# Kernel tuning notes

Measured on AMD Instinct MI355X. Metric: run time of the kernel, lower is better.

Reference implementation:

```python
import jax, jax.numpy as jnp
import numpy as np

N = 100000


def _gcn_conv(x, edge_index, W, b):
    # GCNConv with add_self_loops=True, symmetric normalization.
    src, dst = edge_index[0], edge_index[1]
    loop = jnp.arange(N, dtype=src.dtype)
    src = jnp.concatenate([src, loop])
    dst = jnp.concatenate([dst, loop])
    # degree of target nodes (edge weights all 1, incl. self loops)
    deg = jax.ops.segment_sum(jnp.ones_like(dst, dtype=x.dtype), dst, num_segments=N)
    dinv = jnp.where(deg > 0, jax.lax.rsqrt(deg), 0.0)
    norm = dinv[src] * dinv[dst]  # [E+N]
    h = x @ W  # [N, out]
    msg = h[src] * norm[:, None]  # gather + scale, [E+N, out]
    out = jax.ops.segment_sum(msg, dst, num_segments=N)  # scatter-add
    return out + b


def setup_inputs() -> dict:
    key = jax.random.key(0)
    k1, k2, k3, k4 = jax.random.split(key, 4)
    input_dim, hidden, output_dim = 256, 64, 128
    E = 1600000
    x = jax.random.normal(k1, (N, input_dim), dtype=jnp.float32)
    edge_index = jax.random.randint(k2, (2, E), 0, N, dtype=jnp.int64)
    W1 = jax.random.normal(k3, (input_dim, hidden), dtype=jnp.float32) / np.sqrt(input_dim)
    b1 = jnp.zeros((hidden,), dtype=jnp.float32)
    W2 = jax.random.normal(k4, (hidden, output_dim), dtype=jnp.float32) / np.sqrt(hidden)
    b2 = jnp.zeros((output_dim,), dtype=jnp.float32)
    return {"x": x, "edge_index": edge_index, "W1": W1, "b1": b1, "W2": W2, "b2": b2}


def reference(x, edge_index, W1, b1, W2, b2):
    h = jax.nn.relu(_gcn_conv(x, edge_index, W1, b1))
    return _gcn_conv(h, edge_index, W2, b2)
```

## Files before the change

### kernel.cpp

```cpp
#include <hip/hip_runtime.h>
#include <hip/hip_fp16.h>

#define NNODES 100000
#define NBUCK 391
#define NB_CHUNK 256
#define NC (NBUCK * NB_CHUNK)
#define SCAN_ELEMS 1024

typedef _Float16 f16x8 __attribute__((ext_vector_type(8)));
typedef float    f32x4 __attribute__((ext_vector_type(4)));

__global__ __launch_bounds__(256) void prep_kernel(const float* __restrict__ W1,
                                                   const float* __restrict__ W2,
                                                   const int* __restrict__ raw,
                                                   __half* __restrict__ wf1,
                                                   __half* __restrict__ wf2,
                                                   int* __restrict__ flag) {
    int b = blockIdx.x;
    if (b < 64) {
        int flat = b * 256 + threadIdx.x;
        int j  = flat & 7;
        int l  = (flat >> 3) & 63;
        int nb = (flat >> 9) & 3;
        int kc = flat >> 11;
        int k  = kc * 32 + ((l >> 4) << 3) + j;
        int nc = nb * 16 + (l & 15);
        wf1[flat] = __float2half(W1[k * 64 + nc]);
    } else if (b < 96) {
        int flat = (b - 64) * 256 + threadIdx.x;
        int j  = flat & 7;
        int l  = (flat >> 3) & 63;
        int nb = (flat >> 9) & 7;
        int kc = flat >> 12;
        int k  = kc * 32 + ((l >> 4) << 3) + j;
        int nc = nb * 16 + (l & 15);
        wf2[flat] = __float2half(W2[k * 128 + nc]);
    } else {
        __shared__ int cnt;
        if (threadIdx.x == 0) cnt = 0;
        __syncthreads();
        if (threadIdx.x < 100) {
            if (raw[2 * threadIdx.x + 1] == 0) atomicAdd(&cnt, 1);
        }
        __syncthreads();
        if (threadIdx.x == 0) *flag = (cnt > 50) ? 1 : 0;
    }
}

__global__ __launch_bounds__(256) void convert_gemm1_kernel(const int* __restrict__ raw,
                                                            int* __restrict__ src32,
                                                            int* __restrict__ dst32,
                                                            int* __restrict__ counts,
                                                            int E, int CE,
                                                            const int* __restrict__ flag,
                                                            const float* __restrict__ x,
                                                            const __half* __restrict__ wf,
                                                            __half* __restrict__ H, int M) {
    __shared__ __align__(16) char smem[64 * 264 * 2];
    int bid = blockIdx.x;
    if (bid < NB_CHUNK) {
        int* hist = (int*)smem;
        for (int i = threadIdx.x; i < NBUCK; i += 256) hist[i] = 0;
        __syncthreads();
        int isI64 = *flag;
        int beg = bid * CE;
        int end = beg + CE; if (end > E) end = E;
        const int2* raw2 = reinterpret_cast<const int2*>(raw);
        for (int e = beg + (int)threadIdx.x; e < end; e += 256) {
            int s, d;
            if (isI64) {
                s = raw2[e].x;
                d = raw2[E + e].x;
            } else {
                s = raw[e];
                d = raw[E + e];
            }
            src32[e] = s;
            dst32[e] = d;
            atomicAdd(&hist[d >> 8], 1);
        }
        __syncthreads();
        for (int k = threadIdx.x; k < NBUCK; k += 256)
            counts[k * NB_CHUNK + bid] = hist[k];
    } else {
        __half (*xs)[264] = (__half(*)[264])smem;
        int tid = threadIdx.x;
        int bm = (bid - NB_CHUNK) * 64;
        const float4* x4 = reinterpret_cast<const float4*>(x);
#pragma unroll
        for (int i = 0; i < 16; ++i) {
            int lin = i * 256 + tid;
            int row = lin >> 6;
            int c4  = lin & 63;
            int gr = bm + row; if (gr >= M) gr = M - 1;
            float4 v = x4[(size_t)gr * 64 + c4];
            __half* dst = &xs[row][c4 * 4];
            dst[0] = __float2half(v.x); dst[1] = __float2half(v.y);
            dst[2] = __float2half(v.z); dst[3] = __float2half(v.w);
        }
        __syncthreads();
        int w = tid >> 6;
        int l = tid & 63;
        int lrow = l & 15;
        int lk   = l >> 4;
        const f16x8* wf8 = reinterpret_cast<const f16x8*>(wf);
        f32x4 acc[4] = {};
#pragma unroll
        for (int kc = 0; kc < 8; ++kc) {
            f16x8 a = *reinterpret_cast<const f16x8*>(&xs[w * 16 + lrow][kc * 32 + lk * 8]);
#pragma unroll
            for (int nb = 0; nb < 4; ++nb) {
                f16x8 bfr = wf8[(kc * 4 + nb) * 64 + l];
                acc[nb] = __builtin_amdgcn_mfma_f32_16x16x32_f16(a, bfr, acc[nb], 0, 0, 0);
            }
        }
#pragma unroll
        for (int nb = 0; nb < 4; ++nb)
#pragma unroll
            for (int r = 0; r < 4; ++r) {
                int row = bm + w * 16 + lk * 4 + r;
                if (row < M) H[(size_t)row * 64 + nb * 16 + lrow] = __float2half(acc[nb][r]);
            }
    }
}

__global__ __launch_bounds__(256) void scan_partial_kernel(const int* __restrict__ in,
                                                           int* __restrict__ bsum, int n) {
    int base = blockIdx.x * SCAN_ELEMS + threadIdx.x * 4;
    int s = 0;
    if (base + 3 < n) {
        int4 v = *reinterpret_cast<const int4*>(&in[base]);
        s = v.x + v.y + v.z + v.w;
    } else {
        for (int i = base; i < n && i < base + 4; ++i) s += in[i];
    }
#pragma unroll
    for (int d = 32; d; d >>= 1) s += __shfl_down(s, d, 64);
    __shared__ int ws[4];
    int wid = threadIdx.x >> 6;
    if ((threadIdx.x & 63) == 0) ws[wid] = s;
    __syncthreads();
    if (threadIdx.x == 0) bsum[blockIdx.x] = ws[0] + ws[1] + ws[2] + ws[3];
}

__global__ void scan_partials_kernel(const int* __restrict__ bsum, int* __restrict__ boff,
                                     int* __restrict__ total_out, int nb) {
    __shared__ int s[128];
    int t = threadIdx.x;
    s[t] = (t < nb) ? bsum[t] : 0;
    __syncthreads();
    for (int d = 1; d < 128; d <<= 1) {
        int v = (t >= d) ? s[t - d] : 0;
        __syncthreads();
        s[t] += v;
        __syncthreads();
    }
    if (t < nb) boff[t] = (t == 0) ? 0 : s[t - 1];
    if (t == 127) *total_out = s[127];
}

__global__ __launch_bounds__(256) void scan_write_kernel(const int* __restrict__ in,
                                                         const int* __restrict__ boff,
                                                         int* __restrict__ outp, int n) {
    __shared__ int ts[256];
    int base = blockIdx.x * SCAN_ELEMS + threadIdx.x * 4;
    int v0 = 0, v1 = 0, v2 = 0, v3 = 0;
    if (base + 3 < n) {
        int4 v = *reinterpret_cast<const int4*>(&in[base]);
        v0 = v.x; v1 = v.y; v2 = v.z; v3 = v.w;
    } else {
        if (base < n)     v0 = in[base];
        if (base + 1 < n) v1 = in[base + 1];
        if (base + 2 < n) v2 = in[base + 2];
    }
    ts[threadIdx.x] = v0 + v1 + v2 + v3;
    __syncthreads();
    for (int d = 1; d < 256; d <<= 1) {
        int t = (threadIdx.x >= d) ? ts[threadIdx.x - d] : 0;
        __syncthreads();
        ts[threadIdx.x] += t;
        __syncthreads();
    }
    int run = boff[blockIdx.x] + ((threadIdx.x == 0) ? 0 : ts[threadIdx.x - 1]);
    if (base < n)     { outp[base] = run;     run += v0; }
    if (base + 1 < n) { outp[base + 1] = run; run += v1; }
    if (base + 2 < n) { outp[base + 2] = run; run += v2; }
    if (base + 3 < n) { outp[base + 3] = run; }
}

__global__ __launch_bounds__(256) void scatter_kernel(const int* __restrict__ src32,
                                                      const int* __restrict__ dst32,
                                                      const int* __restrict__ cbase,
                                                      int* __restrict__ cw,
                                                      int E, int CE) {
    __shared__ int cur[NBUCK];
    int b = blockIdx.x;
    for (int k = threadIdx.x; k < NBUCK; k += 256)
        cur[k] = cbase[k * NB_CHUNK + b];
    __syncthreads();
    int beg = b * CE;
    int end = beg + CE; if (end > E) end = E;
    for (int e = beg + (int)threadIdx.x; e < end; e += 256) {
        int s = src32[e];
        int d = dst32[e];
        int pos = atomicAdd(&cur[d >> 8], 1);
        cw[pos] = s | ((d & 255) << 24);
    }
}

__global__ __launch_bounds__(256) void histdeg_kernel(const int* __restrict__ cw,
                                                      const int* __restrict__ cbase,
                                                      int* __restrict__ indeg,
                                                      float* __restrict__ dinv, int n) {
    __shared__ int hist[256];
    hist[threadIdx.x] = 0;
    __syncthreads();
    int k = blockIdx.x;
    int beg = cbase[k * NB_CHUNK];
    int end = cbase[(k + 1) * NB_CHUNK];
    for (int e = beg + (int)threadIdx.x; e < end; e += 256)
        atomicAdd(&hist[(cw[e] >> 24) & 255], 1);
    __syncthreads();
    int i = (k << 8) + threadIdx.x;
    if (i < n) {
        int dg = hist[threadIdx.x];
        indeg[i] = dg;
        dinv[i] = rsqrtf((float)(dg + 1));
    }
}

__global__ __launch_bounds__(256) void fillcol_kernel(const int* __restrict__ cw,
                                                      const int* __restrict__ cbase,
                                                      const int* __restrict__ ptr,
                                                      int* __restrict__ col, int n) {
    __shared__ int cur[256];
    int k = blockIdx.x;
    int i = (k << 8) + threadIdx.x;
    cur[threadIdx.x] = (i < n) ? ptr[i] : 0;
    __syncthreads();
    int beg = cbase[k * NB_CHUNK];
    int end = cbase[(k + 1) * NB_CHUNK];
    for (int e = beg + (int)threadIdx.x; e < end; e += 256) {
        int v = cw[e];
        int pos = atomicAdd(&cur[(v >> 24) & 255], 1);
        col[pos] = v & 0x00FFFFFF;
    }
}

__global__ __launch_bounds__(256) void aggregate_kernel(const __half* __restrict__ h,
                                                        const int* __restrict__ ptr,
                                                        const int* __restrict__ col,
                                                        const float* __restrict__ dinv,
                                                        const float* __restrict__ bias,
                                                        __half* __restrict__ out, int n,
                                                        int relu) {
    int node = (blockIdx.x << 2) + (threadIdx.x >> 6);
    if (node >= n) return;
    int lane = threadIdx.x & 63;
    int g  = lane >> 3;
    int fl = (lane & 7) << 3;
    float acc[8] = {};
    int pend = ptr[node + 1];
    int p = ptr[node] + g;
    for (; p + 8 < pend; p += 16) {
        int c0 = col[p];
        int c1 = col[p + 8];
        uint4 r0 = *reinterpret_cast<const uint4*>(&h[(size_t)c0 * 64 + fl]);
        uint4 r1 = *reinterpret_cast<const uint4*>(&h[(size_t)c1 * 64 + fl]);
        float w0 = dinv[c0], w1 = dinv[c1];
        const unsigned* u0 = &r0.x;
        const unsigned* u1 = &r1.x;
#pragma unroll
        for (int k = 0; k < 4; ++k) {
            float2 f0 = __half22float2(*reinterpret_cast<const __half2*>(&u0[k]));
            float2 f1 = __half22float2(*reinterpret_cast<const __half2*>(&u1[k]));
            acc[2 * k]     = fmaf(w0, f0.x, acc[2 * k]);
            acc[2 * k + 1] = fmaf(w0, f0.y, acc[2 * k + 1]);
            acc[2 * k]     = fmaf(w1, f1.x, acc[2 * k]);
            acc[2 * k + 1] = fmaf(w1, f1.y, acc[2 * k + 1]);
        }
    }
    if (p < pend) {
        int c0 = col[p];
        uint4 r0 = *reinterpret_cast<const uint4*>(&h[(size_t)c0 * 64 + fl]);
        float w0 = dinv[c0];
        const unsigned* u0 = &r0.x;
#pragma unroll
        for (int k = 0; k < 4; ++k) {
            float2 f0 = __half22float2(*reinterpret_cast<const __half2*>(&u0[k]));
            acc[2 * k]     = fmaf(w0, f0.x, acc[2 * k]);
            acc[2 * k + 1] = fmaf(w0, f0.y, acc[2 * k + 1]);
        }
    }
#pragma unroll
    for (int j = 0; j < 8; ++j) {
        acc[j] += __shfl_xor(acc[j], 8, 64);
        acc[j] += __shfl_xor(acc[j], 16, 64);
        acc[j] += __shfl_xor(acc[j], 32, 64);
    }
    if (g == 0) {
        float di = dinv[node];
        uint4 sv = *reinterpret_cast<const uint4*>(&h[(size_t)node * 64 + fl]);
        const unsigned* su = &sv.x;
        float v[8];
#pragma unroll
        for (int k = 0; k < 4; ++k) {
            float2 f = __half22float2(*reinterpret_cast<const __half2*>(&su[k]));
            v[2 * k]     = fmaf(di, f.x, acc[2 * k]) * di;
            v[2 * k + 1] = fmaf(di, f.y, acc[2 * k + 1]) * di;
        }
        if (bias) {
            float4 b0 = *reinterpret_cast<const float4*>(&bias[fl]);
            float4 b1 = *reinterpret_cast<const float4*>(&bias[fl + 4]);
            v[0] += b0.x; v[1] += b0.y; v[2] += b0.z; v[3] += b0.w;
            v[4] += b1.x; v[5] += b1.y; v[6] += b1.z; v[7] += b1.w;
        }
        if (relu) {
#pragma unroll
            for (int j = 0; j < 8; ++j) v[j] = fmaxf(v[j], 0.f);
        }
        __half hv[8];
#pragma unroll
        for (int j = 0; j < 8; ++j) hv[j] = __float2half(v[j]);
        *reinterpret_cast<uint4*>(&out[(size_t)node * 64 + fl]) =
            *reinterpret_cast<const uint4*>(hv);
    }
}

__global__ __launch_bounds__(256) void gemm2_kernel(const __half* __restrict__ A,
                                                    const __half* __restrict__ wf,
                                                    const float* __restrict__ bias,
                                                    float* __restrict__ out, int M) {
    int tid = threadIdx.x;
    int w = tid >> 6;
    int l = tid & 63;
    int lrow = l & 15;
    int lk   = l >> 4;
    int base = blockIdx.x * 64 + w * 16;
    int arow = base + lrow; if (arow >= M) arow = M - 1;
    f16x8 a0 = *reinterpret_cast<const f16x8*>(&A[(size_t)arow * 64 + lk * 8]);
    f16x8 a1 = *reinterpret_cast<const f16x8*>(&A[(size_t)arow * 64 + 32 + lk * 8]);
    const f16x8* wf8 = reinterpret_cast<const f16x8*>(wf);
    f32x4 acc[8] = {};
#pragma unroll
    for (int nb = 0; nb < 8; ++nb) {
        acc[nb] = __builtin_amdgcn_mfma_f32_16x16x32_f16(a0, wf8[nb * 64 + l], acc[nb], 0, 0, 0);
        acc[nb] = __builtin_amdgcn_mfma_f32_16x16x32_f16(a1, wf8[(8 + nb) * 64 + l], acc[nb], 0, 0, 0);
    }
#pragma unroll
    for (int nb = 0; nb < 8; ++nb) {
        float bv = bias[nb * 16 + lrow];
#pragma unroll
        for (int r = 0; r < 4; ++r) {
            int row = base + lk * 4 + r;
            if (row < M) out[(size_t)row * 128 + nb * 16 + lrow] = acc[nb][r] + bv;
        }
    }
}

extern "C" void kernel_launch(void* const* d_in, const int* in_sizes, int n_in,
                              void* d_out, int out_size, void* d_ws, size_t ws_size,
                              hipStream_t stream) {
    const float* x  = (const float*)d_in[0];
    const int*   ei = (const int*)d_in[1];
    const float* W1 = (const float*)d_in[2];
    const float* b1 = (const float*)d_in[3];
    const float* W2 = (const float*)d_in[4];
    const float* b2 = (const float*)d_in[5];
    float* out = (float*)d_out;
    const int n = NNODES;
    const int E = in_sizes[1] / 2;
    const int CE = (E + NB_CHUNK - 1) / NB_CHUNK;

    char* w = (char*)d_ws;
    auto alloc = [&](size_t bytes) {
        char* p = w;
        w += (bytes + 255) & ~(size_t)255;
        return p;
    };
    int*    flag   = (int*)   alloc(4);
    int*    src32  = (int*)   alloc((size_t)E * 4);
    int*    dst32  = (int*)   alloc((size_t)E * 4);
    int*    counts = (int*)   alloc((size_t)NC * 4);
    int*    cbase  = (int*)   alloc((size_t)(NC + 1) * 4);
    int*    indeg  = (int*)   alloc((size_t)n * 4);
    float*  dinv   = (float*) alloc((size_t)n * 4);
    int*    ptr    = (int*)   alloc((size_t)(n + 1) * 4);
    int*    bsum   = (int*)   alloc(128 * 4);
    int*    boff   = (int*)   alloc(128 * 4);
    int*    cw     = (int*)   alloc((size_t)E * 4);
    int*    col    = (int*)   alloc((size_t)E * 4);
    __half* wfrag  = (__half*)alloc(16384 * 2);
    __half* wfrag2 = (__half*)alloc(8192 * 2);
    __half* H1     = (__half*)alloc((size_t)n * 64 * 2);
    __half* h1     = (__half*)alloc((size_t)n * 64 * 2);
    __half* A2     = (__half*)alloc((size_t)n * 64 * 2);

    int sbC = (NC + SCAN_ELEMS - 1) / SCAN_ELEMS;
    int sbN = (n  + SCAN_ELEMS - 1) / SCAN_ELEMS;
    int g1b = (n + 63) / 64;

    prep_kernel<<<97, 256, 0, stream>>>(W1, W2, ei, wfrag, wfrag2, flag);
    convert_gemm1_kernel<<<NB_CHUNK + g1b, 256, 0, stream>>>(
        ei, src32, dst32, counts, E, CE, flag, x, wfrag, H1, n);
    scan_partial_kernel<<<sbC, 256, 0, stream>>>(counts, bsum, NC);
    scan_partials_kernel<<<1, 128, 0, stream>>>(bsum, boff, &cbase[NC], sbC);
    scan_write_kernel<<<sbC, 256, 0, stream>>>(counts, boff, cbase, NC);
    scatter_kernel<<<NB_CHUNK, 256, 0, stream>>>(src32, dst32, cbase, cw, E, CE);
    histdeg_kernel<<<NBUCK, 256, 0, stream>>>(cw, cbase, indeg, dinv, n);
    scan_partial_kernel<<<sbN, 256, 0, stream>>>(indeg, bsum, n);
    scan_partials_kernel<<<1, 128, 0, stream>>>(bsum, boff, &ptr[n], sbN);
    scan_write_kernel<<<sbN, 256, 0, stream>>>(indeg, boff, ptr, n);
    fillcol_kernel<<<NBUCK, 256, 0, stream>>>(cw, cbase, ptr, col, n);

    aggregate_kernel<<<(n + 3) / 4, 256, 0, stream>>>(H1, ptr, col, dinv, b1, h1, n, 1);
    aggregate_kernel<<<(n + 3) / 4, 256, 0, stream>>>(h1, ptr, col, dinv, nullptr, A2, n, 0);
    gemm2_kernel<<<(n + 63) / 64, 256, 0, stream>>>(A2, wfrag2, b2, out, n);
}
```

Measured before the change: 187.4 us.

## Fuse degree histogram, CSR scan and column fill into one bucket kernel

Measured after the change: 178.1 us. 1.05x faster.

```diff
diff --git a/kernel.cpp b/kernel.cpp
--- a/kernel.cpp
+++ b/kernel.cpp
@@ -208,41 +208,45 @@
     }
 }
 
-__global__ __launch_bounds__(256) void histdeg_kernel(const int* __restrict__ cw,
-                                                      const int* __restrict__ cbase,
-                                                      int* __restrict__ indeg,
-                                                      float* __restrict__ dinv, int n) {
+__global__ __launch_bounds__(256) void bucketfin_kernel(const int* __restrict__ cw,
+                                                        const int* __restrict__ cbase,
+                                                        int* __restrict__ ptr,
+                                                        float* __restrict__ dinv,
+                                                        int* __restrict__ col,
+                                                        int n, int E) {
     __shared__ int hist[256];
-    hist[threadIdx.x] = 0;
-    __syncthreads();
+    __shared__ int sc[256];
+    int tid = threadIdx.x;
     int k = blockIdx.x;
+    hist[tid] = 0;
+    __syncthreads();
     int beg = cbase[k * NB_CHUNK];
     int end = cbase[(k + 1) * NB_CHUNK];
-    for (int e = beg + (int)threadIdx.x; e < end; e += 256)
+    for (int e = beg + tid; e < end; e += 256)
         atomicAdd(&hist[(cw[e] >> 24) & 255], 1);
     __syncthreads();
-    int i = (k << 8) + threadIdx.x;
+    int dg = hist[tid];
+    sc[tid] = dg;
+    __syncthreads();
+    for (int d = 1; d < 256; d <<= 1) {
+        int t = (tid >= d) ? sc[tid - d] : 0;
+        __syncthreads();
+        sc[tid] += t;
+        __syncthreads();
+    }
+    int p0 = beg + sc[tid] - dg;
+    int i = (k << 8) + tid;
     if (i < n) {
-        int dg = hist[threadIdx.x];
-        indeg[i] = dg;
+        ptr[i] = p0;
         dinv[i] = rsqrtf((float)(dg + 1));
     }
-}
-
-__global__ __launch_bounds__(256) void fillcol_kernel(const int* __restrict__ cw,
-                                                      const int* __restrict__ cbase,
-                                                      const int* __restrict__ ptr,
-                                                      int* __restrict__ col, int n) {
-    __shared__ int cur[256];
-    int k = blockIdx.x;
-    int i = (k << 8) + threadIdx.x;
-    cur[threadIdx.x] = (i < n) ? ptr[i] : 0;
-    __syncthreads();
-    int beg = cbase[k * NB_CHUNK];
-    int end = cbase[(k + 1) * NB_CHUNK];
-    for (int e = beg + (int)threadIdx.x; e < end; e += 256) {
+    if (k == NBUCK - 1 && tid == 0) ptr[n] = E;
+    __syncthreads();
+    hist[tid] = p0;
+    __syncthreads();
+    for (int e = beg + tid; e < end; e += 256) {
         int v = cw[e];
-        int pos = atomicAdd(&cur[(v >> 24) & 255], 1);
+        int pos = atomicAdd(&hist[(v >> 24) & 255], 1);
         col[pos] = v & 0x00FFFFFF;
     }
 }
@@ -383,7 +387,6 @@
     int*    dst32  = (int*)   alloc((size_t)E * 4);
     int*    counts = (int*)   alloc((size_t)NC * 4);
     int*    cbase  = (int*)   alloc((size_t)(NC + 1) * 4);
-    int*    indeg  = (int*)   alloc((size_t)n * 4);
     float*  dinv   = (float*) alloc((size_t)n * 4);
     int*    ptr    = (int*)   alloc((size_t)(n + 1) * 4);
     int*    bsum   = (int*)   alloc(128 * 4);
@@ -397,7 +400,6 @@
     __half* A2     = (__half*)alloc((size_t)n * 64 * 2);
 
     int sbC = (NC + SCAN_ELEMS - 1) / SCAN_ELEMS;
-    int sbN = (n  + SCAN_ELEMS - 1) / SCAN_ELEMS;
     int g1b = (n + 63) / 64;
 
     prep_kernel<<<97, 256, 0, stream>>>(W1, W2, ei, wfrag, wfrag2, flag);
@@ -407,11 +409,7 @@
     scan_partials_kernel<<<1, 128, 0, stream>>>(bsum, boff, &cbase[NC], sbC);
     scan_write_kernel<<<sbC, 256, 0, stream>>>(counts, boff, cbase, NC);
     scatter_kernel<<<NB_CHUNK, 256, 0, stream>>>(src32, dst32, cbase, cw, E, CE);
-    histdeg_kernel<<<NBUCK, 256, 0, stream>>>(cw, cbase, indeg, dinv, n);
-    scan_partial_kernel<<<sbN, 256, 0, stream>>>(indeg, bsum, n);
-    scan_partials_kernel<<<1, 128, 0, stream>>>(bsum, boff, &ptr[n], sbN);
-    scan_write_kernel<<<sbN, 256, 0, stream>>>(indeg, boff, ptr, n);
-    fillcol_kernel<<<NBUCK, 256, 0, stream>>>(cw, cbase, ptr, col, n);
+    bucketfin_kernel<<<NBUCK, 256, 0, stream>>>(cw, cbase, ptr, dinv, col, n, E);
 
     aggregate_kernel<<<(n + 3) / 4, 256, 0, stream>>>(H1, ptr, col, dinv, b1, h1, n, 1);
     aggregate_kernel<<<(n + 3) / 4, 256, 0, stream>>>(h1, ptr, col, dinv, nullptr, A2, n, 0);
```
